# Performance work log

Measured on AMD Instinct MI355X. Metric: run time of the kernel, lower is better.

Reference implementation:

```python
import jax, jax.numpy as jnp
import numpy as np

NUM_NODES = 50000
NUM_GRAPHS = 64
HIDDEN = 256
F_IN = 256
NUM_EDGES = 800000


def setup_inputs() -> dict:
    key = jax.random.key(0)
    ks = jax.random.split(key, 8)
    x = jax.random.normal(ks[0], (NUM_NODES, F_IN), dtype=jnp.float32)
    edge_index = jax.random.randint(ks[1], (2, NUM_EDGES), 0, NUM_NODES, dtype=jnp.int64)
    batch = jnp.sort(jax.random.randint(ks[2], (NUM_NODES,), 0, NUM_GRAPHS, dtype=jnp.int64))
    # Glorot-ish init for weights, zeros for biases (as PyG GCNConv / Linear defaults)
    s1 = 1.0 / np.sqrt(F_IN)
    s2 = 1.0 / np.sqrt(HIDDEN)
    W1 = jax.random.uniform(ks[3], (F_IN, HIDDEN), jnp.float32, -s1, s1)
    b1 = jnp.zeros((HIDDEN,), jnp.float32)
    W2 = jax.random.uniform(ks[4], (HIDDEN, HIDDEN), jnp.float32, -s2, s2)
    b2 = jnp.zeros((HIDDEN,), jnp.float32)
    W_out = jax.random.uniform(ks[5], (HIDDEN, 1), jnp.float32, -s2, s2)
    b_out = jnp.zeros((1,), jnp.float32)
    return {"x": x, "edge_index": edge_index, "batch": batch,
            "W1": W1, "b1": b1, "W2": W2, "b2": b2,
            "W_out": W_out, "b_out": b_out}


def gcn_conv(x, W, b, src, dst, num_nodes):
    """GCNConv with added self-loops and symmetric D^{-1/2} A D^{-1/2} norm."""
    # degrees over edges incl. self-loops (src/dst already include them)
    deg = jax.ops.segment_sum(jnp.ones_like(src, dtype=x.dtype), dst,
                              num_segments=num_nodes)
    dinv = jax.lax.rsqrt(jnp.maximum(deg, 1e-12))
    norm = dinv[src] * dinv[dst]                       # [E+N]
    h = x @ W                                           # [N, H] dense GEMM
    msg = h[src] * norm[:, None]                        # gather + scale
    out = jax.ops.segment_sum(msg, dst, num_segments=num_nodes)  # scatter-add
    return out + b


def reference(x, edge_index, batch, W1, b1, W2, b2, W_out, b_out):
    n = x.shape[0]
    loops = jnp.arange(n, dtype=edge_index.dtype)
    src = jnp.concatenate([edge_index[0], loops])
    dst = jnp.concatenate([edge_index[1], loops])
    h = jax.nn.relu(gcn_conv(x, W1, b1, src, dst, n))
    h = jax.nn.relu(gcn_conv(h, W2, b2, src, dst, n))
    pooled = jax.ops.segment_sum(h, batch, num_segments=NUM_GRAPHS)  # [G, H]
    return pooled @ W_out + b_out
```

## Files before the change

### kernel.cpp

```cpp
#include <hip/hip_runtime.h>
#include <hip/hip_fp16.h>

#define N_NODES 50000
#define NFEAT   256
#define NGRAPH  64
#define NEDGE   800000
#define NBLK_SCAN 196
#define NBLK_M  196

typedef __attribute__((ext_vector_type(8))) _Float16 half8;
typedef __attribute__((ext_vector_type(2))) _Float16 h2v;
typedef __attribute__((ext_vector_type(4))) float f32x4;
struct alignas(8) US4 { unsigned short x, y, z, w; };

static __device__ __forceinline__ float h2f(unsigned short u) {
    return __half2float(__ushort_as_half(u));
}
static __device__ __forceinline__ unsigned short f2h(float f) {
    return __half_as_ushort(__float2half(f));
}

__global__ void k_count(const int* __restrict__ dst, int* __restrict__ cnt) {
    int e = blockIdx.x * 256 + threadIdx.x;
    if (e < NEDGE) atomicAdd(&cnt[dst[e]], 1);
}

__global__ __launch_bounds__(256) void k_scan1(const int* __restrict__ cnt,
                                               int* __restrict__ row_start,
                                               int* __restrict__ bsum) {
    const int t = threadIdx.x, i = blockIdx.x * 256 + t;
    const int lane = t & 63, w = t >> 6;
    const int c = (i < N_NODES) ? cnt[i] : 0;
    int incl = c;
#pragma unroll
    for (int off = 1; off < 64; off <<= 1) {
        int u = __shfl_up(incl, off, 64);
        if (lane >= off) incl += u;
    }
    __shared__ int wtot[4];
    if (lane == 63) wtot[w] = incl;
    __syncthreads();
    int wbase = 0;
#pragma unroll
    for (int k = 0; k < 4; ++k) wbase += (k < w) ? wtot[k] : 0;
    if (i < N_NODES) row_start[i] = wbase + incl - c;
    if (t == 255) bsum[blockIdx.x] = wbase + incl;
}

__global__ __launch_bounds__(256) void k_scan2(int* __restrict__ bsum) {
    const int t = threadIdx.x, lane = t & 63, w = t >> 6;
    const int c = (t < NBLK_SCAN) ? bsum[t] : 0;
    int incl = c;
#pragma unroll
    for (int off = 1; off < 64; off <<= 1) {
        int u = __shfl_up(incl, off, 64);
        if (lane >= off) incl += u;
    }
    __shared__ int wtot[4];
    if (lane == 63) wtot[w] = incl;
    __syncthreads();
    int wbase = 0;
#pragma unroll
    for (int k = 0; k < 4; ++k) wbase += (k < w) ? wtot[k] : 0;
    if (t < NBLK_SCAN) bsum[t] = wbase + incl - c;
}

__global__ void k_scan3(int* __restrict__ row_start, const int* __restrict__ bsum,
                        int* __restrict__ cnt_cursor, float* __restrict__ dinv) {
    const int i = blockIdx.x * 256 + threadIdx.x;
    if (i >= N_NODES) return;
    const int c = cnt_cursor[i];
    const int start = row_start[i] + bsum[blockIdx.x];
    row_start[i] = start;
    cnt_cursor[i] = start;
    dinv[i] = rsqrtf((float)c + 1.0f);
    if (i == 0) row_start[N_NODES] = NEDGE;
}

__global__ void k_place(const int* __restrict__ src, const int* __restrict__ dst,
                        int* __restrict__ cursor, const float* __restrict__ dinv,
                        unsigned int* __restrict__ csr) {
    int e = blockIdx.x * 256 + threadIdx.x;
    if (e < NEDGE) {
        int s = src[e], d = dst[e];
        float norm = dinv[s] * dinv[d];
        int pos = atomicAdd(&cursor[d], 1);
        csr[pos] = ((unsigned int)f2h(norm) << 16) | (unsigned int)s;
    }
}

__global__ void k_prep_w(const float* __restrict__ W1, const float* __restrict__ W2,
                         unsigned short* __restrict__ w1t, unsigned short* __restrict__ w2t) {
    const int l = blockIdx.x >> 8;
    const int idx = (blockIdx.x & 255) * 256 + threadIdx.x;
    const int n = idx >> 8, k = idx & 255;
    const float* W = l ? W2 : W1;
    unsigned short* wt = l ? w2t : w1t;
    wt[n * 256 + k] = f2h(W[k * 256 + n]);
}

__global__ void k_half_x(const float* __restrict__ x, unsigned short* __restrict__ hx) {
    const int idx = blockIdx.x * 256 + threadIdx.x;
    if (idx >= N_NODES * 32) return;
    const int node = idx >> 5, sub = idx & 31;
    const int half = sub >> 4, fl = sub & 15;
    const float* ap = x + (size_t)node * 256 + half * 128 + fl * 8;
    const float4 p0 = *(const float4*)ap;
    const float4 p1 = *(const float4*)(ap + 4);
    half8 h;
    h[0] = (_Float16)p0.x; h[1] = (_Float16)p0.y;
    h[2] = (_Float16)p0.z; h[3] = (_Float16)p0.w;
    h[4] = (_Float16)p1.x; h[5] = (_Float16)p1.y;
    h[6] = (_Float16)p1.z; h[7] = (_Float16)p1.w;
    *(half8*)(hx + (size_t)half * N_NODES * 128 + (size_t)node * 128 + fl * 8) = h;
}

__global__ __launch_bounds__(512, 4) void k_gemm_mfma(const unsigned short* __restrict__ Ah,
                                                      const unsigned short* __restrict__ Wt,
                                                      unsigned short* __restrict__ Ch, int M) {
    __shared__ unsigned short lds[32768];
    const int t = threadIdx.x;
    const int half = blockIdx.y;
    const int m0 = blockIdx.x * 256;
    const int w = t >> 6, lane = t & 63;
    const int lr = lane & 15, g = lane >> 4;

    {
        const unsigned short* wbase = Wt + (size_t)half * 128 * 256;
#pragma unroll
        for (int it = 0; it < 8; ++it) {
            const int unit = it * 512 + t;
            const int n = unit >> 5;
            const int rem = unit & 31;
            const int ks = rem >> 2, kg = rem & 3;
            const half8 v = *(const half8*)&wbase[n * 256 + rem * 8];
            const int kgx = kg ^ ((n >> 1) & 3);
            *(half8*)&lds[ks * 4096 + n * 32 + kgx * 8] = v;
        }
    }
    __syncthreads();

    const int rbase = m0 + w * 32;
    const unsigned short* Ahh = Ah + (size_t)0;
    unsigned short* Chh = Ch + (size_t)half * (size_t)N_NODES * 128;

    const int row0 = min(rbase + lr, M - 1);
    const int row1 = min(rbase + 16 + lr, M - 1);

    half8 aA[8], aB[8];
#pragma unroll
    for (int ks = 0; ks < 8; ++ks)
        aA[ks] = *(const half8*)(Ahh + (size_t)(ks >> 2) * (size_t)N_NODES * 128 +
                                 (size_t)row0 * 128 + (ks & 3) * 32 + g * 8);
#pragma unroll
    for (int ks = 0; ks < 8; ++ks)
        aB[ks] = *(const half8*)(Ahh + (size_t)(ks >> 2) * (size_t)N_NODES * 128 +
                                 (size_t)row1 * 128 + (ks & 3) * 32 + g * 8);

#define COMPUTE(ROW, SRC)                                                                \
    {                                                                                    \
        f32x4 acc[8] = {};                                                               \
        _Pragma("unroll") for (int ks = 0; ks < 8; ++ks) {                               \
            _Pragma("unroll") for (int ni = 0; ni < 8; ++ni) {                           \
                const int n = ni * 16 + lr;                                              \
                const half8 bf = *(const half8*)&lds[ks * 4096 + n * 32 +                \
                                                     ((g ^ ((n >> 1) & 3)) << 3)];       \
                acc[ni] = __builtin_amdgcn_mfma_f32_16x16x32_f16(bf, SRC[ks],            \
                                                                 acc[ni], 0, 0, 0);      \
            }                                                                            \
        }                                                                                \
        if ((ROW) < M) {                                                                 \
            _Pragma("unroll") for (int ni = 0; ni < 8; ++ni) {                           \
                US4 o;                                                                   \
                o.x = f2h(acc[ni][0]); o.y = f2h(acc[ni][1]);                            \
                o.z = f2h(acc[ni][2]); o.w = f2h(acc[ni][3]);                            \
                *(US4*)(Chh + (size_t)(ROW)*128 + ni * 16 + g * 4) = o;                  \
            }                                                                            \
        }                                                                                \
    }

    const int srow0 = rbase + lr;
    const int srow1 = rbase + 16 + lr;
    COMPUTE(srow0, aA)
    COMPUTE(srow1, aB)
#undef COMPUTE
}

__global__ __launch_bounds__(256) void k_aggregate(const unsigned short* __restrict__ h16,
                                                   const int* __restrict__ row_start,
                                                   const unsigned int* __restrict__ csr,
                                                   const float* __restrict__ dinv,
                                                   const float* __restrict__ bias,
                                                   unsigned short* __restrict__ out) {
    const int wid = blockIdx.x * 4 + (threadIdx.x >> 6);
    if (wid >= 2 * N_NODES) return;
    const int half = (wid >= N_NODES) ? 1 : 0;
    const int node = wid - half * N_NODES;
    const int lane = threadIdx.x & 63;
    const int sub = lane >> 4;
    const int fl = lane & 15;
    const unsigned int* hu = (const unsigned int*)(h16 + (size_t)half * N_NODES * 128);

    float acc[8] = {};
    const int s0 = row_start[node], s1 = row_start[node + 1];
    const unsigned int* row = csr + s0;
    const int n = s1 - s0;

#define EDGEPAIR(EA, EB)                                                              \
    {                                                                                 \
        const unsigned int wnp = __builtin_amdgcn_perm(EB, EA, 0x07060302u);          \
        const h2v wn2 = __builtin_bit_cast(h2v, wnp);                                 \
        const uint4 va = *(const uint4*)(hu + (size_t)((EA)&0xffffu) * 64 + fl * 4);  \
        const uint4 vb = *(const uint4*)(hu + (size_t)((EB)&0xffffu) * 64 + fl * 4);  \
        unsigned int plo, phi;                                                        \
        plo = __builtin_amdgcn_perm(vb.x, va.x, 0x05040100u);                         \
        phi = __builtin_amdgcn_perm(vb.x, va.x, 0x07060302u);                         \
        acc[0] = __builtin_amdgcn_fdot2(__builtin_bit_cast(h2v, plo), wn2, acc[0], false); \
        acc[1] = __builtin_amdgcn_fdot2(__builtin_bit_cast(h2v, phi), wn2, acc[1], false); \
        plo = __builtin_amdgcn_perm(vb.y, va.y, 0x05040100u);                         \
        phi = __builtin_amdgcn_perm(vb.y, va.y, 0x07060302u);                         \
        acc[2] = __builtin_amdgcn_fdot2(__builtin_bit_cast(h2v, plo), wn2, acc[2], false); \
        acc[3] = __builtin_amdgcn_fdot2(__builtin_bit_cast(h2v, phi), wn2, acc[3], false); \
        plo = __builtin_amdgcn_perm(vb.z, va.z, 0x05040100u);                         \
        phi = __builtin_amdgcn_perm(vb.z, va.z, 0x07060302u);                         \
        acc[4] = __builtin_amdgcn_fdot2(__builtin_bit_cast(h2v, plo), wn2, acc[4], false); \
        acc[5] = __builtin_amdgcn_fdot2(__builtin_bit_cast(h2v, phi), wn2, acc[5], false); \
        plo = __builtin_amdgcn_perm(vb.w, va.w, 0x05040100u);                         \
        phi = __builtin_amdgcn_perm(vb.w, va.w, 0x07060302u);                         \
        acc[6] = __builtin_amdgcn_fdot2(__builtin_bit_cast(h2v, plo), wn2, acc[6], false); \
        acc[7] = __builtin_amdgcn_fdot2(__builtin_bit_cast(h2v, phi), wn2, acc[7], false); \
    }

    const int nfull = n & ~7;
    int j = 0;
    for (; j < nfull; j += 8) {
        const unsigned int ea = row[j + sub * 2];
        const unsigned int eb = row[j + sub * 2 + 1];
        EDGEPAIR(ea, eb)
    }
    if (j < n) {
        const int ia = j + sub * 2, ib = ia + 1;
        const unsigned int ea = (ia < n) ? row[ia] : 0u;
        const unsigned int eb = (ib < n) ? row[ib] : 0u;
        EDGEPAIR(ea, eb)
    }
#undef EDGEPAIR

#pragma unroll
    for (int i = 0; i < 8; ++i) {
        acc[i] += __shfl_xor(acc[i], 16, 64);
        acc[i] += __shfl_xor(acc[i], 32, 64);
    }

    if (sub == 0) {
        const float dd = dinv[node];
        const float ws = dd * dd;
        const uint4 sh = *(const uint4*)(hu + (size_t)node * 64 + fl * 4);
        const float4 b0 = *(const float4*)(bias + half * 128 + fl * 8);
        const float4 b1 = *(const float4*)(bias + half * 128 + fl * 8 + 4);
        float r[8];
        r[0] = fmaf(h2f((unsigned short)(sh.x & 0xffff)), ws, acc[0]) + b0.x;
        r[1] = fmaf(h2f((unsigned short)(sh.x >> 16)),    ws, acc[1]) + b0.y;
        r[2] = fmaf(h2f((unsigned short)(sh.y & 0xffff)), ws, acc[2]) + b0.z;
        r[3] = fmaf(h2f((unsigned short)(sh.y >> 16)),    ws, acc[3]) + b0.w;
        r[4] = fmaf(h2f((unsigned short)(sh.z & 0xffff)), ws, acc[4]) + b1.x;
        r[5] = fmaf(h2f((unsigned short)(sh.z >> 16)),    ws, acc[5]) + b1.y;
        r[6] = fmaf(h2f((unsigned short)(sh.w & 0xffff)), ws, acc[6]) + b1.z;
        r[7] = fmaf(h2f((unsigned short)(sh.w >> 16)),    ws, acc[7]) + b1.w;
#pragma unroll
        for (int i = 0; i < 8; ++i) r[i] = fmaxf(r[i], 0.f);
        uint4 o;
        o.x = (unsigned int)f2h(r[0]) | ((unsigned int)f2h(r[1]) << 16);
        o.y = (unsigned int)f2h(r[2]) | ((unsigned int)f2h(r[3]) << 16);
        o.z = (unsigned int)f2h(r[4]) | ((unsigned int)f2h(r[5]) << 16);
        o.w = (unsigned int)f2h(r[6]) | ((unsigned int)f2h(r[7]) << 16);
        *(uint4*)((unsigned int*)(out + (size_t)half * N_NODES * 128) +
                  (size_t)node * 64 + fl * 4) = o;
    }
}

__global__ void k_pool(const unsigned short* __restrict__ h2, const int* __restrict__ batch,
                       float* __restrict__ pooled) {
    const int strip = blockIdx.x * 2 + (threadIdx.x >> 7);
    const int tf = threadIdx.x & 127;
    const int f = tf * 2;
    const unsigned short* base = h2 + (size_t)(f >> 7) * N_NODES * 128 + (f & 127);
    const int n0 = strip * 40, n1 = n0 + 40;
    int g = batch[n0];
    float ax = 0.f, ay = 0.f;
    for (int n = n0; n < n1; ++n) {
        const int bg = batch[n];
        if (bg != g) {
            unsafeAtomicAdd(&pooled[g * NFEAT + f], ax);
            unsafeAtomicAdd(&pooled[g * NFEAT + f + 1], ay);
            ax = ay = 0.f;
            g = bg;
        }
        const unsigned int u = *(const unsigned int*)(base + (size_t)n * 128);
        ax += h2f((unsigned short)(u & 0xffff));
        ay += h2f((unsigned short)(u >> 16));
    }
    unsafeAtomicAdd(&pooled[g * NFEAT + f], ax);
    unsafeAtomicAdd(&pooled[g * NFEAT + f + 1], ay);
}

__global__ void k_final(const float* __restrict__ pooled, const float* __restrict__ Wout,
                        const float* __restrict__ bout, float* __restrict__ out) {
    const int g = blockIdx.x, t = threadIdx.x;
    float v = pooled[g * NFEAT + t] * Wout[t];
#pragma unroll
    for (int off = 32; off > 0; off >>= 1) v += __shfl_down(v, off, 64);
    __shared__ float sred[4];
    if ((t & 63) == 0) sred[t >> 6] = v;
    __syncthreads();
    if (t == 0) out[g] = sred[0] + sred[1] + sred[2] + sred[3] + bout[0];
}

extern "C" void kernel_launch(void* const* d_in, const int* in_sizes, int n_in,
                              void* d_out, int out_size, void* d_ws, size_t ws_size,
                              hipStream_t stream) {
    const float* x     = (const float*)d_in[0];
    const int*   ei    = (const int*)d_in[1];
    const int*   batch = (const int*)d_in[2];
    const float* W1    = (const float*)d_in[3];
    const float* b1    = (const float*)d_in[4];
    const float* W2    = (const float*)d_in[5];
    const float* b2    = (const float*)d_in[6];
    const float* Wout  = (const float*)d_in[7];
    const float* bout  = (const float*)d_in[8];
    float* out = (float*)d_out;

    const int* srcp = ei;
    const int* dstp = ei + NEDGE;

    const size_t NE128 = (size_t)N_NODES * 128;
    unsigned short* hA = (unsigned short*)d_ws;
    unsigned short* hB = hA + 2 * NE128;
    unsigned short* hX = hB + 2 * NE128;
    float* dinv      = (float*)(hX + 2 * NE128);
    float* pooled    = dinv + N_NODES;
    int*   cnt       = (int*)(pooled + NGRAPH * NFEAT);
    int*   row_start = cnt + N_NODES;
    int*   bsum      = row_start + N_NODES + 3;
    unsigned int* csr = (unsigned int*)(bsum + 256);
    unsigned short* w1t = (unsigned short*)(csr + NEDGE);
    unsigned short* w2t = w1t + 65536;

    const int nblk_edges = (NEDGE + 255) / 256;

    hipMemsetAsync(cnt, 0, N_NODES * sizeof(int), stream);
    k_count<<<nblk_edges, 256, 0, stream>>>(dstp, cnt);
    k_scan1<<<NBLK_SCAN, 256, 0, stream>>>(cnt, row_start, bsum);
    k_scan2<<<1, 256, 0, stream>>>(bsum);
    k_scan3<<<NBLK_SCAN, 256, 0, stream>>>(row_start, bsum, cnt, dinv);
    k_place<<<nblk_edges, 256, 0, stream>>>(srcp, dstp, cnt, dinv, csr);

    k_prep_w<<<512, 256, 0, stream>>>(W1, W2, w1t, w2t);
    k_half_x<<<(N_NODES * 32 + 255) / 256, 256, 0, stream>>>(x, hX);

    const dim3 ggrid(NBLK_M, 2);
    const int agg_grid = (2 * N_NODES + 3) / 4;

    k_gemm_mfma<<<ggrid, 512, 0, stream>>>(hX, w1t, hA, N_NODES);
    k_aggregate<<<agg_grid, 256, 0, stream>>>(hA, row_start, csr, dinv, b1, hB);

    k_gemm_mfma<<<ggrid, 512, 0, stream>>>(hB, w2t, hA, N_NODES);
    k_aggregate<<<agg_grid, 256, 0, stream>>>(hA, row_start, csr, dinv, b2, hB);

    hipMemsetAsync(pooled, 0, NGRAPH * NFEAT * sizeof(float), stream);
    k_pool<<<625, 256, 0, stream>>>(hB, batch, pooled);
    k_final<<<NGRAPH, 256, 0, stream>>>(pooled, Wout, bout, out);
}
```

Baseline: 299.5 us.

## Keep GEMM weights in registers and record edge rank to avoid second atomic pass

```diff
diff --git a/kernel.cpp b/kernel.cpp
--- a/kernel.cpp
+++ b/kernel.cpp
@@ -6,7 +6,6 @@
 #define NGRAPH  64
 #define NEDGE   800000
 #define NBLK_SCAN 196
-#define NBLK_M  196
 
 typedef __attribute__((ext_vector_type(8))) _Float16 half8;
 typedef __attribute__((ext_vector_type(2))) _Float16 h2v;
@@ -20,9 +19,10 @@
     return __half_as_ushort(__float2half(f));
 }
 
-__global__ void k_count(const int* __restrict__ dst, int* __restrict__ cnt) {
+__global__ void k_count(const int* __restrict__ dst, int* __restrict__ cnt,
+                        int* __restrict__ rank) {
     int e = blockIdx.x * 256 + threadIdx.x;
-    if (e < NEDGE) atomicAdd(&cnt[dst[e]], 1);
+    if (e < NEDGE) rank[e] = atomicAdd(&cnt[dst[e]], 1);
 }
 
 __global__ __launch_bounds__(256) void k_scan1(const int* __restrict__ cnt,
@@ -66,26 +66,23 @@
 }
 
 __global__ void k_scan3(int* __restrict__ row_start, const int* __restrict__ bsum,
-                        int* __restrict__ cnt_cursor, float* __restrict__ dinv) {
+                        const int* __restrict__ cnt, float* __restrict__ dinv) {
     const int i = blockIdx.x * 256 + threadIdx.x;
     if (i >= N_NODES) return;
-    const int c = cnt_cursor[i];
-    const int start = row_start[i] + bsum[blockIdx.x];
-    row_start[i] = start;
-    cnt_cursor[i] = start;
-    dinv[i] = rsqrtf((float)c + 1.0f);
+    row_start[i] += bsum[blockIdx.x];
+    dinv[i] = rsqrtf((float)cnt[i] + 1.0f);
     if (i == 0) row_start[N_NODES] = NEDGE;
 }
 
 __global__ void k_place(const int* __restrict__ src, const int* __restrict__ dst,
-                        int* __restrict__ cursor, const float* __restrict__ dinv,
-                        unsigned int* __restrict__ csr) {
+                        const int* __restrict__ rank, const int* __restrict__ row_start,
+                        const float* __restrict__ dinv, unsigned int* __restrict__ csr) {
     int e = blockIdx.x * 256 + threadIdx.x;
     if (e < NEDGE) {
         int s = src[e], d = dst[e];
         float norm = dinv[s] * dinv[d];
-        int pos = atomicAdd(&cursor[d], 1);
-        csr[pos] = ((unsigned int)f2h(norm) << 16) | (unsigned int)s;
+        csr[row_start[d] + rank[e]] =
+            ((unsigned int)f2h(norm) << 16) | (unsigned int)s;
     }
 }
 
@@ -115,74 +112,71 @@
     *(half8*)(hx + (size_t)half * N_NODES * 128 + (size_t)node * 128 + fl * 8) = h;
 }
 
-__global__ __launch_bounds__(512, 4) void k_gemm_mfma(const unsigned short* __restrict__ Ah,
-                                                      const unsigned short* __restrict__ Wt,
-                                                      unsigned short* __restrict__ Ch, int M) {
-    __shared__ unsigned short lds[32768];
+__global__ __launch_bounds__(512, 3) void k_gemm_ws(const unsigned short* __restrict__ Ah,
+                                                    const unsigned short* __restrict__ Wt,
+                                                    unsigned short* __restrict__ Ch, int M) {
     const int t = threadIdx.x;
-    const int half = blockIdx.y;
-    const int m0 = blockIdx.x * 256;
     const int w = t >> 6, lane = t & 63;
     const int lr = lane & 15, g = lane >> 4;
-
-    {
-        const unsigned short* wbase = Wt + (size_t)half * 128 * 256;
-#pragma unroll
-        for (int it = 0; it < 8; ++it) {
-            const int unit = it * 512 + t;
-            const int n = unit >> 5;
-            const int rem = unit & 31;
-            const int ks = rem >> 2, kg = rem & 3;
-            const half8 v = *(const half8*)&wbase[n * 256 + rem * 8];
-            const int kgx = kg ^ ((n >> 1) & 3);
-            *(half8*)&lds[ks * 4096 + n * 32 + kgx * 8] = v;
-        }
-    }
-    __syncthreads();
-
-    const int rbase = m0 + w * 32;
-    const unsigned short* Ahh = Ah + (size_t)0;
-    unsigned short* Chh = Ch + (size_t)half * (size_t)N_NODES * 128;
-
-    const int row0 = min(rbase + lr, M - 1);
-    const int row1 = min(rbase + 16 + lr, M - 1);
+    const int c0 = w * 32;
+    const int m0 = blockIdx.x * 128;
+
+    half8 bf[2][8];
+#pragma unroll
+    for (int ni = 0; ni < 2; ++ni)
+#pragma unroll
+        for (int ks = 0; ks < 8; ++ks)
+            bf[ni][ks] = *(const half8*)&Wt[(size_t)(c0 + ni * 16 + lr) * 256 + ks * 32 + g * 8];
 
     half8 aA[8], aB[8];
-#pragma unroll
-    for (int ks = 0; ks < 8; ++ks)
-        aA[ks] = *(const half8*)(Ahh + (size_t)(ks >> 2) * (size_t)N_NODES * 128 +
-                                 (size_t)row0 * 128 + (ks & 3) * 32 + g * 8);
-#pragma unroll
-    for (int ks = 0; ks < 8; ++ks)
-        aB[ks] = *(const half8*)(Ahh + (size_t)(ks >> 2) * (size_t)N_NODES * 128 +
-                                 (size_t)row1 * 128 + (ks & 3) * 32 + g * 8);
-
-#define COMPUTE(ROW, SRC)                                                                \
-    {                                                                                    \
-        f32x4 acc[8] = {};                                                               \
-        _Pragma("unroll") for (int ks = 0; ks < 8; ++ks) {                               \
-            _Pragma("unroll") for (int ni = 0; ni < 8; ++ni) {                           \
-                const int n = ni * 16 + lr;                                              \
-                const half8 bf = *(const half8*)&lds[ks * 4096 + n * 32 +                \
-                                                     ((g ^ ((n >> 1) & 3)) << 3)];       \
-                acc[ni] = __builtin_amdgcn_mfma_f32_16x16x32_f16(bf, SRC[ks],            \
-                                                                 acc[ni], 0, 0, 0);      \
-            }                                                                            \
-        }                                                                                \
-        if ((ROW) < M) {                                                                 \
-            _Pragma("unroll") for (int ni = 0; ni < 8; ++ni) {                           \
-                US4 o;                                                                   \
-                o.x = f2h(acc[ni][0]); o.y = f2h(acc[ni][1]);                            \
-                o.z = f2h(acc[ni][2]); o.w = f2h(acc[ni][3]);                            \
-                *(US4*)(Chh + (size_t)(ROW)*128 + ni * 16 + g * 4) = o;                  \
-            }                                                                            \
-        }                                                                                \
-    }
-
-    const int srow0 = rbase + lr;
-    const int srow1 = rbase + 16 + lr;
-    COMPUTE(srow0, aA)
-    COMPUTE(srow1, aB)
+
+#define LOADA(C, DST)                                                                     \
+    {                                                                                     \
+        const int row = min(m0 + (C) * 16 + lr, M - 1);                                   \
+        _Pragma("unroll") for (int ks = 0; ks < 8; ++ks)                                  \
+            DST[ks] = *(const half8*)(Ah + (size_t)(ks >> 2) * (size_t)N_NODES * 128 +    \
+                                      (size_t)row * 128 + (ks & 3) * 32 + g * 8);         \
+    }
+#define COMPUTE(C, SRC)                                                                   \
+    {                                                                                     \
+        f32x4 acc0 = {}, acc1 = {};                                                       \
+        _Pragma("unroll") for (int ks = 0; ks < 8; ++ks) {                                \
+            acc0 = __builtin_amdgcn_mfma_f32_16x16x32_f16(bf[0][ks], SRC[ks], acc0, 0, 0, 0); \
+            acc1 = __builtin_amdgcn_mfma_f32_16x16x32_f16(bf[1][ks], SRC[ks], acc1, 0, 0, 0); \
+        }                                                                                 \
+        const int row = m0 + (C) * 16 + lr;                                               \
+        if (row < M) {                                                                    \
+            US4 o0, o1;                                                                   \
+            o0.x = f2h(acc0[0]); o0.y = f2h(acc0[1]);                                     \
+            o0.z = f2h(acc0[2]); o0.w = f2h(acc0[3]);                                     \
+            o1.x = f2h(acc1[0]); o1.y = f2h(acc1[1]);                                     \
+            o1.z = f2h(acc1[2]); o1.w = f2h(acc1[3]);                                     \
+            const int col0 = c0 + g * 4;                                                  \
+            const int col1 = c0 + 16 + g * 4;                                             \
+            *(US4*)(Ch + (size_t)(col0 >> 7) * (size_t)N_NODES * 128 +                    \
+                    (size_t)row * 128 + (col0 & 127)) = o0;                               \
+            *(US4*)(Ch + (size_t)(col1 >> 7) * (size_t)N_NODES * 128 +                    \
+                    (size_t)row * 128 + (col1 & 127)) = o1;                               \
+        }                                                                                 \
+    }
+
+    LOADA(0, aA)
+    LOADA(1, aB)
+    COMPUTE(0, aA)
+    LOADA(2, aA)
+    COMPUTE(1, aB)
+    LOADA(3, aB)
+    COMPUTE(2, aA)
+    LOADA(4, aA)
+    COMPUTE(3, aB)
+    LOADA(5, aB)
+    COMPUTE(4, aA)
+    LOADA(6, aA)
+    COMPUTE(5, aB)
+    LOADA(7, aB)
+    COMPUTE(6, aA)
+    COMPUTE(7, aB)
+#undef LOADA
 #undef COMPUTE
 }
 
@@ -343,28 +337,29 @@
     int*   row_start = cnt + N_NODES;
     int*   bsum      = row_start + N_NODES + 3;
     unsigned int* csr = (unsigned int*)(bsum + 256);
-    unsigned short* w1t = (unsigned short*)(csr + NEDGE);
+    int*   rank      = (int*)(csr + NEDGE);
+    unsigned short* w1t = (unsigned short*)(rank + NEDGE);
     unsigned short* w2t = w1t + 65536;
 
     const int nblk_edges = (NEDGE + 255) / 256;
 
     hipMemsetAsync(cnt, 0, N_NODES * sizeof(int), stream);
-    k_count<<<nblk_edges, 256, 0, stream>>>(dstp, cnt);
+    k_count<<<nblk_edges, 256, 0, stream>>>(dstp, cnt, rank);
     k_scan1<<<NBLK_SCAN, 256, 0, stream>>>(cnt, row_start, bsum);
     k_scan2<<<1, 256, 0, stream>>>(bsum);
     k_scan3<<<NBLK_SCAN, 256, 0, stream>>>(row_start, bsum, cnt, dinv);
-    k_place<<<nblk_edges, 256, 0, stream>>>(srcp, dstp, cnt, dinv, csr);
+    k_place<<<nblk_edges, 256, 0, stream>>>(srcp, dstp, rank, row_start, dinv, csr);
 
     k_prep_w<<<512, 256, 0, stream>>>(W1, W2, w1t, w2t);
     k_half_x<<<(N_NODES * 32 + 255) / 256, 256, 0, stream>>>(x, hX);
 
-    const dim3 ggrid(NBLK_M, 2);
+    const int ggrid = 391;
     const int agg_grid = (2 * N_NODES + 3) / 4;
 
-    k_gemm_mfma<<<ggrid, 512, 0, stream>>>(hX, w1t, hA, N_NODES);
+    k_gemm_ws<<<ggrid, 512, 0, stream>>>(hX, w1t, hA, N_NODES);
     k_aggregate<<<agg_grid, 256, 0, stream>>>(hA, row_start, csr, dinv, b1, hB);
 
-    k_gemm_mfma<<<ggrid, 512, 0, stream>>>(hB, w2t, hA, N_NODES);
+    k_gemm_ws<<<ggrid, 512, 0, stream>>>(hB, w2t, hA, N_NODES);
     k_aggregate<<<agg_grid, 256, 0, stream>>>(hA, row_start, csr, dinv, b2, hB);
 
     hipMemsetAsync(pooled, 0, NGRAPH * NFEAT * sizeof(float), stream);
```

Result: no change. 301.0 us (+0.5%).
